# Performance work log

Measured on AMD Instinct MI355X. Metric: run time of the kernel, lower is better.

## Reference

```python
import jax, jax.numpy as jnp
import numpy as np

N = 10000
E = 160000
H = 4
NEG_SLOPE = 0.2


def _edge_softmax(e, dst):
    # e: [E, H] logits; softmax over edges sharing the same dst node
    m = jax.ops.segment_max(e, dst, num_segments=N)          # [N, H]
    m = jnp.where(jnp.isfinite(m), m, 0.0)
    ex = jnp.exp(e - m[dst])                                  # [E, H]
    den = jax.ops.segment_sum(ex, dst, num_segments=N)       # [N, H]
    return ex / (den[dst] + 1e-9)


def _gat_layer(x, src, dst, W, al, ar, resW, edge=None, We=None, ae=None):
    # x: [N, Fin]; W: [Fin, H, D]; al/ar/ae: [H, D]; resW: [Fin, D]
    feat = jnp.einsum('ni,ihd->nhd', x, W)                    # [N, H, D]
    el = jnp.einsum('nhd,hd->nh', feat, al)                   # [N, H]
    er = jnp.einsum('nhd,hd->nh', feat, ar)                   # [N, H]
    e = el[src] + er[dst]                                     # [E, H]
    if edge is not None:
        ef = jnp.einsum('ei,ihd->ehd', edge, We)              # [E, H, D]
        e = e + jnp.einsum('ehd,hd->eh', ef, ae)
    e = jax.nn.leaky_relu(e, NEG_SLOPE)
    alpha = _edge_softmax(e, dst)                             # [E, H]
    msg = feat[src] * alpha[:, :, None]                       # [E, H, D]
    out = jax.ops.segment_sum(msg, dst, num_segments=N)      # [N, H, D]
    return out.mean(axis=1) + x @ resW                        # [N, D]


def setup_inputs() -> dict:
    key = jax.random.key(0)
    ks = jax.random.split(key, 24)
    node_in, edge_in, hid, out = 128, 64, 128, 256
    s = 0.1
    d = {
        'node_feats': jax.random.normal(ks[0], (N, node_in), jnp.float32),
        'edge_feats': jax.random.normal(ks[1], (E, edge_in), jnp.float32),
        'src': jax.random.randint(ks[2], (E,), 0, N, jnp.int32),
        'dst': jax.random.randint(ks[3], (E,), 0, N, jnp.int32),
        # conv1 (with edge feats): node_in -> hid
        'W1':  s * jax.random.normal(ks[4],  (node_in, H, hid), jnp.float32),
        'We1': s * jax.random.normal(ks[5],  (edge_in, H, hid), jnp.float32),
        'al1': s * jax.random.normal(ks[6],  (H, hid), jnp.float32),
        'ar1': s * jax.random.normal(ks[7],  (H, hid), jnp.float32),
        'ae1': s * jax.random.normal(ks[8],  (H, hid), jnp.float32),
        'res1': s * jax.random.normal(ks[9], (node_in, hid), jnp.float32),
        # conv2: hid -> hid
        'W2':  s * jax.random.normal(ks[10], (hid, H, hid), jnp.float32),
        'al2': s * jax.random.normal(ks[11], (H, hid), jnp.float32),
        'ar2': s * jax.random.normal(ks[12], (H, hid), jnp.float32),
        'res2': s * jax.random.normal(ks[13], (hid, hid), jnp.float32),
        # conv3: hid -> hid
        'W3':  s * jax.random.normal(ks[14], (hid, H, hid), jnp.float32),
        'al3': s * jax.random.normal(ks[15], (H, hid), jnp.float32),
        'ar3': s * jax.random.normal(ks[16], (H, hid), jnp.float32),
        'res3': s * jax.random.normal(ks[17], (hid, hid), jnp.float32),
        # conv4: hid -> out
        'W4':  s * jax.random.normal(ks[18], (hid, H, out), jnp.float32),
        'al4': s * jax.random.normal(ks[19], (H, out), jnp.float32),
        'ar4': s * jax.random.normal(ks[20], (H, out), jnp.float32),
        'res4': s * jax.random.normal(ks[21], (hid, out), jnp.float32),
    }
    return d


def reference(node_feats, edge_feats, src, dst,
              W1, We1, al1, ar1, ae1, res1,
              W2, al2, ar2, res2,
              W3, al3, ar3, res3,
              W4, al4, ar4, res4):
    h = jax.nn.relu(_gat_layer(node_feats, src, dst, W1, al1, ar1, res1,
                               edge=edge_feats, We=We1, ae=ae1))
    h = jax.nn.relu(_gat_layer(h, src, dst, W2, al2, ar2, res2))
    h = jax.nn.relu(_gat_layer(h, src, dst, W3, al3, ar3, res3))
    h = jax.nn.relu(_gat_layer(h, src, dst, W4, al4, ar4, res4))
    return h
```

## Files before the change

### kernel.cpp

```cpp
#include <hip/hip_runtime.h>

#define NN 10000
#define EE 160000

typedef __attribute__((ext_vector_type(8))) short bf16x8;
typedef __attribute__((ext_vector_type(4))) float f32x4;
typedef __attribute__((ext_vector_type(2))) float f32x2;

__device__ __forceinline__ float b2f(unsigned short s) {
    union { unsigned u; float f; } v; v.u = ((unsigned)s) << 16; return v.f;
}
__device__ __forceinline__ short f2b(float f) {
    union { float f; unsigned u; } v; v.f = f;
    unsigned r = v.u + 0x7FFF + ((v.u >> 16) & 1);
    return (short)(r >> 16);
}
__device__ __forceinline__ unsigned char f2q(float f) {
    return (unsigned char)(__builtin_amdgcn_cvt_pk_fp8_f32(f, f, 0, false) & 0xFF);
}

__global__ __launch_bounds__(256) void hist_kernel(const int* __restrict__ dst,
                                                   int* __restrict__ counts, int E) {
    int e = blockIdx.x * 256 + threadIdx.x;
    if (e < E) atomicAdd(&counts[dst[e]], 1);
}

__global__ __launch_bounds__(256) void scan_kernel(const int* __restrict__ counts,
                                                   int* __restrict__ off,
                                                   int* __restrict__ cur, int n) {
    __shared__ int buf[NN];
    __shared__ int part[256];
    int tid = threadIdx.x;
    for (int j = tid; j < n; j += 256) buf[j] = counts[j];
    __syncthreads();
    int chunk = (n + 255) / 256;
    int lo = tid * chunk; if (lo > n) lo = n;
    int hi = lo + chunk;  if (hi > n) hi = n;
    int s = 0;
    for (int i = lo; i < hi; ++i) s += buf[i];
    part[tid] = s;
    __syncthreads();
    for (int o = 1; o < 256; o <<= 1) {
        int v = (tid >= o) ? part[tid - o] : 0;
        __syncthreads();
        part[tid] += v;
        __syncthreads();
    }
    int run = (tid == 0) ? 0 : part[tid - 1];
    for (int i = lo; i < hi; ++i) { int c = buf[i]; buf[i] = run; run += c; }
    __syncthreads();
    for (int j = tid; j < n; j += 256) { int v = buf[j]; off[j] = v; cur[j] = v; }
    if (tid == 255) off[n] = part[255];
}

__global__ __launch_bounds__(256) void fill_extra(const int* __restrict__ src,
                                                  const int* __restrict__ dst,
                                                  int* __restrict__ cur,
                                                  const float* __restrict__ ef,
                                                  const float* __restrict__ vbuf,
                                                  int* __restrict__ ssrc,
                                                  float* __restrict__ extra, int E) {
    __shared__ float vs[256];
    vs[threadIdx.x] = vbuf[threadIdx.x];
    __syncthreads();
    int e = blockIdx.x * 256 + threadIdx.x;
    if (e >= E) return;
    int p = atomicAdd(&cur[dst[e]], 1);
    ssrc[p] = src[e];
    float a0 = 0.f, a1 = 0.f, a2 = 0.f, a3 = 0.f;
    const float4* e4 = (const float4*)(ef + (size_t)e * 64);
    #pragma unroll
    for (int c = 0; c < 16; ++c) {
        float4 x = e4[c];
        int b = c * 16;
        a0 += x.x * vs[b + 0] + x.y * vs[b + 4] + x.z * vs[b + 8] + x.w * vs[b + 12];
        a1 += x.x * vs[b + 1] + x.y * vs[b + 5] + x.z * vs[b + 9] + x.w * vs[b + 13];
        a2 += x.x * vs[b + 2] + x.y * vs[b + 6] + x.z * vs[b + 10] + x.w * vs[b + 14];
        a3 += x.x * vs[b + 3] + x.y * vs[b + 7] + x.z * vs[b + 11] + x.w * vs[b + 15];
    }
    float4 o; o.x = a0; o.y = a1; o.z = a2; o.w = a3;
    *(float4*)(extra + (size_t)p * 4) = o;
}

struct PrepParams {
    const float* tsrc[8];
    short* tdst[8];
    int tN[8];
    int tshift[8];
    int tcum4[9];
    const float* W[4]; const float* al[4]; const float* ar[4];
    short* Wc[4]; int Dl[4]; int base[4];
    const float* We1; const float* ae1; float* vbuf;
    const float* node_feats; short* xb;
    int* counts;
    int bWA, bV, bC, bZ;
};
__global__ __launch_bounds__(256) void prep_kernel(PrepParams P) {
    int blk = blockIdx.x, tid = threadIdx.x;
    if (blk < P.bWA) {
        int t = blk * 256 + tid;
        if (t >= P.tcum4[8]) return;
        int i = 0;
        #pragma unroll
        for (int j = 1; j < 8; ++j) i += (t >= P.tcum4[j]);
        int local = t - P.tcum4[i];
        int N = P.tN[i], sh = P.tshift[i];
        int k = local >> (sh - 2);
        int nq = local & ((N >> 2) - 1);
        float4 v = *(const float4*)(P.tsrc[i] + (size_t)k * N + nq * 4);
        short* d = P.tdst[i] + (size_t)nq * 4 * 128 + k;
        d[0] = f2b(v.x); d[128] = f2b(v.y); d[256] = f2b(v.z); d[384] = f2b(v.w);
    } else if (blk < P.bV) {
        int bl = blk - P.bWA;
        int l = bl >> 7, within = bl & 127;
        int wv = tid >> 6, ln = tid & 63;
        int wid = within * 4 + wv;
        int k = wid >> 2, h = wid & 3;
        int D = P.Dl[l];
        const float* w = P.W[l] + ((size_t)k * 4 + h) * D;
        const float* a = P.al[l] + (size_t)h * D;
        const float* r = P.ar[l] + (size_t)h * D;
        float sa, sr;
        if (D == 128) {
            float2 w2 = ((const float2*)w)[ln];
            float2 a2 = ((const float2*)a)[ln];
            float2 r2 = ((const float2*)r)[ln];
            sa = w2.x * a2.x + w2.y * a2.y;
            sr = w2.x * r2.x + w2.y * r2.y;
        } else {
            float4 w4 = ((const float4*)w)[ln];
            float4 a4 = ((const float4*)a)[ln];
            float4 r4 = ((const float4*)r)[ln];
            sa = w4.x * a4.x + w4.y * a4.y + w4.z * a4.z + w4.w * a4.w;
            sr = w4.x * r4.x + w4.y * r4.y + w4.z * r4.z + w4.w * r4.w;
        }
        #pragma unroll
        for (int o = 32; o; o >>= 1) { sa += __shfl_xor(sa, o); sr += __shfl_xor(sr, o); }
        if (ln == 0) {
            P.Wc[l][(size_t)(P.base[l] + h) * 128 + k]     = f2b(sa);
            P.Wc[l][(size_t)(P.base[l] + 4 + h) * 128 + k] = f2b(sr);
        }
    } else if (blk < P.bC) {
        int bl = blk - P.bV;
        int wv = tid >> 6, ln = tid & 63;
        int i = bl * 4 + wv;
        #pragma unroll
        for (int h = 0; h < 4; ++h) {
            const float* w = P.We1 + ((size_t)i * 4 + h) * 128;
            const float* a = P.ae1 + (size_t)h * 128;
            float2 w2 = ((const float2*)w)[ln];
            float2 a2 = ((const float2*)a)[ln];
            float s = w2.x * a2.x + w2.y * a2.y;
            #pragma unroll
            for (int o = 32; o; o >>= 1) s += __shfl_xor(s, o);
            if (ln == 0) P.vbuf[i * 4 + h] = s;
        }
    } else if (blk < P.bZ) {
        int t = (blk - P.bC) * 256 + tid;
        if (t < NN * 32) {
            float4 v = ((const float4*)P.node_feats)[t];
            uint2 pk;
            pk.x = (unsigned short)f2b(v.x) | ((unsigned)(unsigned short)f2b(v.y) << 16);
            pk.y = (unsigned short)f2b(v.z) | ((unsigned)(unsigned short)f2b(v.w) << 16);
            ((uint2*)P.xb)[t] = pk;
        }
    } else {
        int t = (blk - P.bZ) * 256 + tid;
        if (t < NN / 4) ((int4*)P.counts)[t] = make_int4(0, 0, 0, 0);
    }
}

template <int D>
__global__ __launch_bounds__(256) void gemm_fused(const short* __restrict__ A,
                                                  const short* __restrict__ Bt,
                                                  unsigned char* __restrict__ featq,
                                                  float* __restrict__ y,
                                                  float* __restrict__ elr,
                                                  int M) {
    constexpr int HD = 4 * D;
    int wave = threadIdx.x >> 6, lane = threadIdx.x & 63;
    int m0 = blockIdx.y * 64;
    int n0 = blockIdx.x * 64 + wave * 16;
    int r = lane & 15, quad = lane >> 4;
    f32x4 acc[4] = {};
    const short* bp = Bt + (size_t)(n0 + r) * 128 + quad * 8;
    #pragma unroll
    for (int k0 = 0; k0 < 128; k0 += 32) {
        bf16x8 bfrag = *(const bf16x8*)(bp + k0);
        #pragma unroll
        for (int mt = 0; mt < 4; ++mt) {
            int gm = m0 + mt * 16 + r;
            bf16x8 afrag = {};
            if (gm < M) afrag = *(const bf16x8*)(A + (size_t)gm * 128 + k0 + quad * 8);
            acc[mt] = __builtin_amdgcn_mfma_f32_16x16x32_bf16(afrag, bfrag, acc[mt], 0, 0, 0);
        }
    }
    int col = n0 + r;
    #pragma unroll
    for (int mt = 0; mt < 4; ++mt) {
        #pragma unroll
        for (int rr = 0; rr < 4; ++rr) {
            int gm = m0 + mt * 16 + quad * 4 + rr;
            if (gm >= M) continue;
            float v = acc[mt][rr];
            if (col < HD)              featq[(size_t)gm * HD + col] = f2q(v);
            else if (col < HD + D)     y[(size_t)gm * D + (col - HD)] = v;
            else if (col < HD + D + 8) elr[(size_t)gm * 8 + (col - HD - D)] = v;
        }
    }
}

__device__ __forceinline__ void accum16q(float* a, uint4 v, float w) {
    f32x2 p;
    p = __builtin_amdgcn_cvt_pk_f32_fp8(v.x, false); a[0] += w * p.x; a[1] += w * p.y;
    p = __builtin_amdgcn_cvt_pk_f32_fp8(v.x, true);  a[2] += w * p.x; a[3] += w * p.y;
    p = __builtin_amdgcn_cvt_pk_f32_fp8(v.y, false); a[4] += w * p.x; a[5] += w * p.y;
    p = __builtin_amdgcn_cvt_pk_f32_fp8(v.y, true);  a[6] += w * p.x; a[7] += w * p.y;
    p = __builtin_amdgcn_cvt_pk_f32_fp8(v.z, false); a[8] += w * p.x; a[9] += w * p.y;
    p = __builtin_amdgcn_cvt_pk_f32_fp8(v.z, true);  a[10] += w * p.x; a[11] += w * p.y;
    p = __builtin_amdgcn_cvt_pk_f32_fp8(v.w, false); a[12] += w * p.x; a[13] += w * p.y;
    p = __builtin_amdgcn_cvt_pk_f32_fp8(v.w, true);  a[14] += w * p.x; a[15] += w * p.y;
}

__device__ __forceinline__ float hsel(int h, float s0, float s1, float s2, float s3) {
    return h == 0 ? s0 : h == 1 ? s1 : h == 2 ? s2 : s3;
}

__device__ __forceinline__ void gather128(int T, int deg, int g, int h, int sidx,
                                          float e0, float e1, float e2, float e3,
                                          const unsigned char* __restrict__ basep,
                                          float acc[16]) {
    int it = 0;
    for (; it + 4 <= T; it += 4) {
        int j0 = 2 * it + g, j1 = j0 + 2, j2 = j0 + 4, j3 = j0 + 6;
        int c0 = j0 < deg ? j0 : deg - 1;
        int c1 = j1 < deg ? j1 : deg - 1;
        int c2 = j2 < deg ? j2 : deg - 1;
        int c3 = j3 < deg ? j3 : deg - 1;
        float m0 = j0 < deg ? 1.f : 0.f, m1 = j1 < deg ? 1.f : 0.f;
        float m2 = j2 < deg ? 1.f : 0.f, m3 = j3 < deg ? 1.f : 0.f;
        int s0 = __shfl(sidx, c0), s1 = __shfl(sidx, c1);
        int s2 = __shfl(sidx, c2), s3 = __shfl(sidx, c3);
        uint4 v0 = *(const uint4*)(basep + (size_t)s0 * 512);
        uint4 v1 = *(const uint4*)(basep + (size_t)s1 * 512);
        uint4 v2 = *(const uint4*)(basep + (size_t)s2 * 512);
        uint4 v3 = *(const uint4*)(basep + (size_t)s3 * 512);
        float w0 = hsel(h, __shfl(e0, c0), __shfl(e1, c0), __shfl(e2, c0), __shfl(e3, c0)) * m0;
        float w1 = hsel(h, __shfl(e0, c1), __shfl(e1, c1), __shfl(e2, c1), __shfl(e3, c1)) * m1;
        float w2 = hsel(h, __shfl(e0, c2), __shfl(e1, c2), __shfl(e2, c2), __shfl(e3, c2)) * m2;
        float w3 = hsel(h, __shfl(e0, c3), __shfl(e1, c3), __shfl(e2, c3), __shfl(e3, c3)) * m3;
        accum16q(acc, v0, w0); accum16q(acc, v1, w1);
        accum16q(acc, v2, w2); accum16q(acc, v3, w3);
    }
    for (; it < T; ++it) {
        int j0 = 2 * it + g;
        int c0 = j0 < deg ? j0 : deg - 1;
        float m0 = j0 < deg ? 1.f : 0.f;
        int s0 = __shfl(sidx, c0);
        uint4 v0 = *(const uint4*)(basep + (size_t)s0 * 512);
        float w0 = hsel(h, __shfl(e0, c0), __shfl(e1, c0), __shfl(e2, c0), __shfl(e3, c0)) * m0;
        accum16q(acc, v0, w0);
    }
}

__device__ __forceinline__ void gather256(int T, int deg, int half, int h, int sidx,
                                          float e0, float e1, float e2, float e3,
                                          const unsigned char* __restrict__ basep,
                                          float acc[16]) {
    int it = 0;
    for (; it + 4 <= T; it += 4) {
        int j0 = 2 * it + half, j1 = j0 + 2, j2 = j0 + 4, j3 = j0 + 6;
        int c0 = j0 < deg ? j0 : deg - 1;
        int c1 = j1 < deg ? j1 : deg - 1;
        int c2 = j2 < deg ? j2 : deg - 1;
        int c3 = j3 < deg ? j3 : deg - 1;
        float m0 = j0 < deg ? 1.f : 0.f, m1 = j1 < deg ? 1.f : 0.f;
        float m2 = j2 < deg ? 1.f : 0.f, m3 = j3 < deg ? 1.f : 0.f;
        int s0 = __shfl(sidx, c0), s1 = __shfl(sidx, c1);
        int s2 = __shfl(sidx, c2), s3 = __shfl(sidx, c3);
        uint4 v0 = *(const uint4*)(basep + (size_t)s0 * 1024);
        uint4 v1 = *(const uint4*)(basep + (size_t)s1 * 1024);
        uint4 v2 = *(const uint4*)(basep + (size_t)s2 * 1024);
        uint4 v3 = *(const uint4*)(basep + (size_t)s3 * 1024);
        float w0 = hsel(h, __shfl(e0, c0), __shfl(e1, c0), __shfl(e2, c0), __shfl(e3, c0)) * m0;
        float w1 = hsel(h, __shfl(e0, c1), __shfl(e1, c1), __shfl(e2, c1), __shfl(e3, c1)) * m1;
        float w2 = hsel(h, __shfl(e0, c2), __shfl(e1, c2), __shfl(e2, c2), __shfl(e3, c2)) * m2;
        float w3 = hsel(h, __shfl(e0, c3), __shfl(e1, c3), __shfl(e2, c3), __shfl(e3, c3)) * m3;
        accum16q(acc, v0, w0); accum16q(acc, v1, w1);
        accum16q(acc, v2, w2); accum16q(acc, v3, w3);
    }
    for (; it < T; ++it) {
        int j0 = 2 * it + half;
        int c0 = j0 < deg ? j0 : deg - 1;
        float m0 = j0 < deg ? 1.f : 0.f;
        int s0 = __shfl(sidx, c0);
        uint4 v0 = *(const uint4*)(basep + (size_t)s0 * 1024);
        float w0 = hsel(h, __shfl(e0, c0), __shfl(e1, c0), __shfl(e2, c0), __shfl(e3, c0)) * m0;
        accum16q(acc, v0, w0);
    }
}

#define WAVE_MAX4(m0,m1,m2,m3)                                              \
    _Pragma("unroll")                                                       \
    for (int o = 32; o; o >>= 1) {                                          \
        m0 = fmaxf(m0, __shfl_xor(m0, o)); m1 = fmaxf(m1, __shfl_xor(m1, o));\
        m2 = fmaxf(m2, __shfl_xor(m2, o)); m3 = fmaxf(m3, __shfl_xor(m3, o));\
    }
#define WAVE_SUM4(s0,s1,s2,s3)                                              \
    _Pragma("unroll")                                                       \
    for (int o = 32; o; o >>= 1) {                                          \
        s0 += __shfl_xor(s0, o); s1 += __shfl_xor(s1, o);                   \
        s2 += __shfl_xor(s2, o); s3 += __shfl_xor(s3, o);                   \
    }

template <bool HAS_EXTRA>
__global__ __launch_bounds__(256) void gat128(const unsigned char* __restrict__ featq,
                                              const float* __restrict__ elr,
                                              const float* __restrict__ extra,
                                              const int* __restrict__ ssrc,
                                              const int* __restrict__ off,
                                              const float* __restrict__ yres,
                                              short* __restrict__ ybf) {
    int wv = threadIdx.x >> 6, ln = threadIdx.x & 63;
    int n = blockIdx.x * 4 + wv;
    int r0 = off[n], deg = off[n + 1] - r0;
    int g = ln >> 5, l5 = ln & 31;
    int h = l5 >> 3;
    float4 erv = *(const float4*)(elr + (size_t)n * 8 + 4);
    float acc[16];
    #pragma unroll
    for (int i = 0; i < 16; ++i) acc[i] = 0.f;
    float sc0, sc1, sc2, sc3;
    const unsigned char* basep = featq + l5 * 16;

    auto logits = [&](int idx, float& a0, float& a1, float& a2, float& a3) {
        int s = ssrc[idx];
        float4 elv = *(const float4*)(elr + (size_t)s * 8);
        a0 = elv.x + erv.x; a1 = elv.y + erv.y; a2 = elv.z + erv.z; a3 = elv.w + erv.w;
        if (HAS_EXTRA) {
            float4 exv = *(const float4*)(extra + (size_t)idx * 4);
            a0 += exv.x; a1 += exv.y; a2 += exv.z; a3 += exv.w;
        }
        a0 = a0 > 0.f ? a0 : 0.2f * a0;
        a1 = a1 > 0.f ? a1 : 0.2f * a1;
        a2 = a2 > 0.f ? a2 : 0.2f * a2;
        a3 = a3 > 0.f ? a3 : 0.2f * a3;
        return s;
    };

    if (deg <= 64) {
        int sidx = 0;
        float a0 = -1e30f, a1 = -1e30f, a2 = -1e30f, a3 = -1e30f;
        if (ln < deg) sidx = logits(r0 + ln, a0, a1, a2, a3);
        float m0 = a0, m1 = a1, m2 = a2, m3 = a3;
        WAVE_MAX4(m0, m1, m2, m3)
        float e0 = 0.f, e1 = 0.f, e2 = 0.f, e3 = 0.f;
        if (ln < deg) {
            e0 = __expf(a0 - m0); e1 = __expf(a1 - m1);
            e2 = __expf(a2 - m2); e3 = __expf(a3 - m3);
        }
        float s0 = e0, s1 = e1, s2 = e2, s3 = e3;
        WAVE_SUM4(s0, s1, s2, s3)
        sc0 = 0.25f / (s0 + 1e-9f); sc1 = 0.25f / (s1 + 1e-9f);
        sc2 = 0.25f / (s2 + 1e-9f); sc3 = 0.25f / (s3 + 1e-9f);
        gather128((deg + 1) >> 1, deg, g, h, sidx, e0, e1, e2, e3, basep, acc);
    } else {
        float m0 = -1e30f, m1 = -1e30f, m2 = -1e30f, m3 = -1e30f;
        for (int b = 0; b < deg; b += 64) {
            float a0 = -1e30f, a1 = -1e30f, a2 = -1e30f, a3 = -1e30f;
            if (b + ln < deg) logits(r0 + b + ln, a0, a1, a2, a3);
            m0 = fmaxf(m0, a0); m1 = fmaxf(m1, a1); m2 = fmaxf(m2, a2); m3 = fmaxf(m3, a3);
        }
        WAVE_MAX4(m0, m1, m2, m3)
        float s0 = 0.f, s1 = 0.f, s2 = 0.f, s3 = 0.f;
        for (int b = 0; b < deg; b += 64) {
            float a0, a1, a2, a3;
            if (b + ln < deg) {
                logits(r0 + b + ln, a0, a1, a2, a3);
                s0 += __expf(a0 - m0); s1 += __expf(a1 - m1);
                s2 += __expf(a2 - m2); s3 += __expf(a3 - m3);
            }
        }
        WAVE_SUM4(s0, s1, s2, s3)
        sc0 = 0.25f / (s0 + 1e-9f); sc1 = 0.25f / (s1 + 1e-9f);
        sc2 = 0.25f / (s2 + 1e-9f); sc3 = 0.25f / (s3 + 1e-9f);
        for (int b = 0; b < deg; b += 64) {
            int sidx = 0;
            float e0 = 0.f, e1 = 0.f, e2 = 0.f, e3 = 0.f;
            if (b + ln < deg) {
                float a0, a1, a2, a3;
                sidx = logits(r0 + b + ln, a0, a1, a2, a3);
                e0 = __expf(a0 - m0); e1 = __expf(a1 - m1);
                e2 = __expf(a2 - m2); e3 = __expf(a3 - m3);
            }
            int cnt = deg - b; if (cnt > 64) cnt = 64;
            gather128((cnt + 1) >> 1, cnt, g, h, sidx, e0, e1, e2, e3, basep, acc);
        }
    }

    float scl = hsel(h, sc0, sc1, sc2, sc3);
    float t[16];
    #pragma unroll
    for (int i = 0; i < 16; ++i) {
        float v = acc[i] * scl;
        v += __shfl_xor(v, 32);
        v += __shfl_xor(v, 8);
        v += __shfl_xor(v, 16);
        t[i] = v;
    }
    if (ln < 8) {
        int d0 = ln * 16;
        const float* yr = yres + (size_t)n * 128 + d0;
        unsigned pk[8];
        #pragma unroll
        for (int q = 0; q < 8; ++q) {
            float ya = yr[2 * q], yb = yr[2 * q + 1];
            float o0 = fmaxf(ya + t[2 * q], 0.f);
            float o1 = fmaxf(yb + t[2 * q + 1], 0.f);
            pk[q] = (unsigned short)f2b(o0) | ((unsigned)(unsigned short)f2b(o1) << 16);
        }
        uint4 pa, pb;
        pa.x = pk[0]; pa.y = pk[1]; pa.z = pk[2]; pa.w = pk[3];
        pb.x = pk[4]; pb.y = pk[5]; pb.z = pk[6]; pb.w = pk[7];
        *(uint4*)(ybf + (size_t)n * 128 + d0) = pa;
        *(uint4*)(ybf + (size_t)n * 128 + d0 + 8) = pb;
    }
}

__global__ __launch_bounds__(256) void gat256(const unsigned char* __restrict__ featq,
                                              const float* __restrict__ elr,
                                              const int* __restrict__ ssrc,
                                              const int* __restrict__ off,
                                              const float* __restrict__ yres,
                                              float* __restrict__ yout) {
    __shared__ float red[2][256];
    int wv = threadIdx.x >> 6, ln = threadIdx.x & 63;
    int slot = wv >> 1, half = wv & 1;
    int n = blockIdx.x * 2 + slot;
    int r0 = off[n], deg = off[n + 1] - r0;
    int h = ln >> 4;
    float4 erv = *(const float4*)(elr + (size_t)n * 8 + 4);
    float acc[16];
    #pragma unroll
    for (int i = 0; i < 16; ++i) acc[i] = 0.f;
    float sc0, sc1, sc2, sc3;
    const unsigned char* basep = featq + ln * 16;

    auto logits = [&](int idx, float& a0, float& a1, float& a2, float& a3) {
        int s = ssrc[idx];
        float4 elv = *(const float4*)(elr + (size_t)s * 8);
        a0 = elv.x + erv.x; a1 = elv.y + erv.y; a2 = elv.z + erv.z; a3 = elv.w + erv.w;
        a0 = a0 > 0.f ? a0 : 0.2f * a0;
        a1 = a1 > 0.f ? a1 : 0.2f * a1;
        a2 = a2 > 0.f ? a2 : 0.2f * a2;
        a3 = a3 > 0.f ? a3 : 0.2f * a3;
        return s;
    };

    if (deg <= 64) {
        int sidx = 0;
        float a0 = -1e30f, a1 = -1e30f, a2 = -1e30f, a3 = -1e30f;
        if (ln < deg) sidx = logits(r0 + ln, a0, a1, a2, a3);
        float m0 = a0, m1 = a1, m2 = a2, m3 = a3;
        WAVE_MAX4(m0, m1, m2, m3)
        float e0 = 0.f, e1 = 0.f, e2 = 0.f, e3 = 0.f;
        if (ln < deg) {
            e0 = __expf(a0 - m0); e1 = __expf(a1 - m1);
            e2 = __expf(a2 - m2); e3 = __expf(a3 - m3);
        }
        float s0 = e0, s1 = e1, s2 = e2, s3 = e3;
        WAVE_SUM4(s0, s1, s2, s3)
        sc0 = 0.25f / (s0 + 1e-9f); sc1 = 0.25f / (s1 + 1e-9f);
        sc2 = 0.25f / (s2 + 1e-9f); sc3 = 0.25f / (s3 + 1e-9f);
        gather256((deg + 1) >> 1, deg, half, h, sidx, e0, e1, e2, e3, basep, acc);
    } else {
        float m0 = -1e30f, m1 = -1e30f, m2 = -1e30f, m3 = -1e30f;
        for (int b = 0; b < deg; b += 64) {
            float a0 = -1e30f, a1 = -1e30f, a2 = -1e30f, a3 = -1e30f;
            if (b + ln < deg) logits(r0 + b + ln, a0, a1, a2, a3);
            m0 = fmaxf(m0, a0); m1 = fmaxf(m1, a1); m2 = fmaxf(m2, a2); m3 = fmaxf(m3, a3);
        }
        WAVE_MAX4(m0, m1, m2, m3)
        float s0 = 0.f, s1 = 0.f, s2 = 0.f, s3 = 0.f;
        for (int b = 0; b < deg; b += 64) {
            float a0, a1, a2, a3;
            if (b + ln < deg) {
                logits(r0 + b + ln, a0, a1, a2, a3);
                s0 += __expf(a0 - m0); s1 += __expf(a1 - m1);
                s2 += __expf(a2 - m2); s3 += __expf(a3 - m3);
            }
        }
        WAVE_SUM4(s0, s1, s2, s3)
        sc0 = 0.25f / (s0 + 1e-9f); sc1 = 0.25f / (s1 + 1e-9f);
        sc2 = 0.25f / (s2 + 1e-9f); sc3 = 0.25f / (s3 + 1e-9f);
        for (int b = 0; b < deg; b += 64) {
            int sidx = 0;
            float e0 = 0.f, e1 = 0.f, e2 = 0.f, e3 = 0.f;
            if (b + ln < deg) {
                float a0, a1, a2, a3;
                sidx = logits(r0 + b + ln, a0, a1, a2, a3);
                e0 = __expf(a0 - m0); e1 = __expf(a1 - m1);
                e2 = __expf(a2 - m2); e3 = __expf(a3 - m3);
            }
            int cnt = deg - b; if (cnt > 64) cnt = 64;
            gather256((cnt + 1) >> 1, cnt, half, h, sidx, e0, e1, e2, e3, basep, acc);
        }
    }

    float scl = hsel(h, sc0, sc1, sc2, sc3);
    float t[16];
    #pragma unroll
    for (int i = 0; i < 16; ++i) {
        float v = acc[i] * scl;
        v += __shfl_xor(v, 16);
        v += __shfl_xor(v, 32);
        t[i] = v;
    }
    if (half == 1 && ln < 16) {
        #pragma unroll
        for (int i = 0; i < 16; ++i) red[slot][ln * 16 + i] = t[i];
    }
    __syncthreads();
    if (half == 0 && ln < 16) {
        int d0 = ln * 16;
        const float* yr = yres + (size_t)n * 256 + d0;
        float* yo = yout + (size_t)n * 256 + d0;
        #pragma unroll
        for (int q = 0; q < 4; ++q) {
            float4 ya = *(const float4*)(yr + 4 * q);
            float4 ov;
            ov.x = fmaxf(ya.x + t[4 * q + 0] + red[slot][d0 + 4 * q + 0], 0.f);
            ov.y = fmaxf(ya.y + t[4 * q + 1] + red[slot][d0 + 4 * q + 1], 0.f);
            ov.z = fmaxf(ya.z + t[4 * q + 2] + red[slot][d0 + 4 * q + 2], 0.f);
            ov.w = fmaxf(ya.w + t[4 * q + 3] + red[slot][d0 + 4 * q + 3], 0.f);
            *(float4*)(yo + 4 * q) = ov;
        }
    }
}

extern "C" void kernel_launch(void* const* d_in, const int* in_sizes, int n_in,
                              void* d_out, int out_size, void* d_ws, size_t ws_size,
                              hipStream_t stream) {
    const float* node_feats = (const float*)d_in[0];
    const float* edge_feats = (const float*)d_in[1];
    const int*   src        = (const int*)d_in[2];
    const int*   dst        = (const int*)d_in[3];
    const float* W1   = (const float*)d_in[4];
    const float* We1  = (const float*)d_in[5];
    const float* al1  = (const float*)d_in[6];
    const float* ar1  = (const float*)d_in[7];
    const float* ae1  = (const float*)d_in[8];
    const float* res1 = (const float*)d_in[9];
    const float* W2   = (const float*)d_in[10];
    const float* al2  = (const float*)d_in[11];
    const float* ar2  = (const float*)d_in[12];
    const float* res2 = (const float*)d_in[13];
    const float* W3   = (const float*)d_in[14];
    const float* al3  = (const float*)d_in[15];
    const float* ar3  = (const float*)d_in[16];
    const float* res3 = (const float*)d_in[17];
    const float* W4   = (const float*)d_in[18];
    const float* al4  = (const float*)d_in[19];
    const float* ar4  = (const float*)d_in[20];
    const float* res4 = (const float*)d_in[21];

    char* ws = (char*)d_ws;
    auto alloc = [&](size_t bytes) -> char* {
        char* p = ws;
        ws += (bytes + 255) & ~(size_t)255;
        return p;
    };
    int*   counts  = (int*)alloc((size_t)NN * 4);
    int*   offsets = (int*)alloc((size_t)(NN + 1) * 4);
    int*   cursor  = (int*)alloc((size_t)(NN + 1) * 4);
    int*   ssrc    = (int*)alloc((size_t)EE * 4);
    unsigned char* featq = (unsigned char*)alloc((size_t)NN * 1024);
    float* xA      = (float*)alloc((size_t)NN * 128 * 4);
    short* xb      = (short*)alloc((size_t)NN * 128 * 2);
    float* elr     = (float*)alloc((size_t)NN * 8 * 4);
    float* extra   = (float*)alloc((size_t)EE * 4 * 4);
    float* vbuf    = (float*)alloc(1024);
    short* Wc1     = (short*)alloc((size_t)704 * 128 * 2);
    short* Wc2     = (short*)alloc((size_t)704 * 128 * 2);
    short* Wc3     = (short*)alloc((size_t)704 * 128 * 2);
    short* Wc4     = (short*)alloc((size_t)1344 * 128 * 2);

    PrepParams P;
    P.tsrc[0] = W1;   P.tdst[0] = Wc1;              P.tN[0] = 512;  P.tshift[0] = 9;
    P.tsrc[1] = W2;   P.tdst[1] = Wc2;              P.tN[1] = 512;  P.tshift[1] = 9;
    P.tsrc[2] = W3;   P.tdst[2] = Wc3;              P.tN[2] = 512;  P.tshift[2] = 9;
    P.tsrc[3] = W4;   P.tdst[3] = Wc4;              P.tN[3] = 1024; P.tshift[3] = 10;
    P.tsrc[4] = res1; P.tdst[4] = Wc1 + 512 * 128;  P.tN[4] = 128;  P.tshift[4] = 7;
    P.tsrc[5] = res2; P.tdst[5] = Wc2 + 512 * 128;  P.tN[5] = 128;  P.tshift[5] = 7;
    P.tsrc[6] = res3; P.tdst[6] = Wc3 + 512 * 128;  P.tN[6] = 128;  P.tshift[6] = 7;
    P.tsrc[7] = res4; P.tdst[7] = Wc4 + 1024 * 128; P.tN[7] = 256;  P.tshift[7] = 8;
    P.tcum4[0] = 0;
    for (int i = 0; i < 8; ++i) P.tcum4[i + 1] = P.tcum4[i] + P.tN[i] * 128 / 4;
    P.W[0] = W1; P.W[1] = W2; P.W[2] = W3; P.W[3] = W4;
    P.al[0] = al1; P.al[1] = al2; P.al[2] = al3; P.al[3] = al4;
    P.ar[0] = ar1; P.ar[1] = ar2; P.ar[2] = ar3; P.ar[3] = ar4;
    P.Wc[0] = Wc1; P.Wc[1] = Wc2; P.Wc[2] = Wc3; P.Wc[3] = Wc4;
    P.Dl[0] = 128; P.Dl[1] = 128; P.Dl[2] = 128; P.Dl[3] = 256;
    P.base[0] = 640; P.base[1] = 640; P.base[2] = 640; P.base[3] = 1280;
    P.We1 = We1; P.ae1 = ae1; P.vbuf = vbuf;
    P.node_feats = node_feats; P.xb = xb;
    P.counts = counts;
    P.bWA = (P.tcum4[8] + 255) / 256;
    P.bV  = P.bWA + 512;
    P.bC  = P.bV + 16;
    P.bZ  = P.bC + (NN * 32 + 255) / 256;
    int nblk = P.bZ + (NN / 4 + 255) / 256;
    prep_kernel<<<nblk, 256, 0, stream>>>(P);

    hist_kernel<<<(EE + 255) / 256, 256, 0, stream>>>(dst, counts, EE);
    scan_kernel<<<1, 256, 0, stream>>>(counts, offsets, cursor, NN);
    fill_extra<<<(EE + 255) / 256, 256, 0, stream>>>(src, dst, cursor, edge_feats,
                                                     vbuf, ssrc, extra, EE);

    float* out = (float*)d_out;
    dim3 g128(11, (NN + 63) / 64);
    dim3 g256(21, (NN + 63) / 64);
    int gs128 = NN / 4;
    int gs256 = NN / 2;

    gemm_fused<128><<<g128, 256, 0, stream>>>(xb, Wc1, featq, xA, elr, NN);
    gat128<true><<<gs128, 256, 0, stream>>>(featq, elr, extra, ssrc, offsets, xA, xb);
    gemm_fused<128><<<g128, 256, 0, stream>>>(xb, Wc2, featq, xA, elr, NN);
    gat128<false><<<gs128, 256, 0, stream>>>(featq, elr, nullptr, ssrc, offsets, xA, xb);
    gemm_fused<128><<<g128, 256, 0, stream>>>(xb, Wc3, featq, xA, elr, NN);
    gat128<false><<<gs128, 256, 0, stream>>>(featq, elr, nullptr, ssrc, offsets, xA, xb);
    gemm_fused<256><<<g256, 256, 0, stream>>>(xb, Wc4, featq, out, elr, NN);
    gat256<<<gs256, 256, 0, stream>>>(featq, elr, ssrc, offsets, out, out);
}
```

Baseline: 364.5 us.

## Fuse histogram into first GEMM, widen per-node gather across waves, register scan

```diff
diff --git a/kernel.cpp b/kernel.cpp
--- a/kernel.cpp
+++ b/kernel.cpp
@@ -19,25 +19,27 @@
     return (unsigned char)(__builtin_amdgcn_cvt_pk_fp8_f32(f, f, 0, false) & 0xFF);
 }
 
-__global__ __launch_bounds__(256) void hist_kernel(const int* __restrict__ dst,
-                                                   int* __restrict__ counts, int E) {
-    int e = blockIdx.x * 256 + threadIdx.x;
-    if (e < E) atomicAdd(&counts[dst[e]], 1);
-}
-
 __global__ __launch_bounds__(256) void scan_kernel(const int* __restrict__ counts,
                                                    int* __restrict__ off,
                                                    int* __restrict__ cur, int n) {
-    __shared__ int buf[NN];
     __shared__ int part[256];
     int tid = threadIdx.x;
-    for (int j = tid; j < n; j += 256) buf[j] = counts[j];
-    __syncthreads();
-    int chunk = (n + 255) / 256;
-    int lo = tid * chunk; if (lo > n) lo = n;
-    int hi = lo + chunk;  if (hi > n) hi = n;
+    int lo = tid * 40;
+    int4 r[10];
     int s = 0;
-    for (int i = lo; i < hi; ++i) s += buf[i];
+    #pragma unroll
+    for (int q = 0; q < 10; ++q) {
+        int idx = lo + q * 4;
+        int4 v = make_int4(0, 0, 0, 0);
+        if (idx + 3 < n) v = *(const int4*)(counts + idx);
+        else if (idx < n) {
+            v.x = counts[idx];
+            v.y = (idx + 1 < n) ? counts[idx + 1] : 0;
+            v.z = (idx + 2 < n) ? counts[idx + 2] : 0;
+        }
+        r[q] = v;
+        s += v.x + v.y + v.z + v.w;
+    }
     part[tid] = s;
     __syncthreads();
     for (int o = 1; o < 256; o <<= 1) {
@@ -46,10 +48,22 @@
         part[tid] += v;
         __syncthreads();
     }
-    int run = (tid == 0) ? 0 : part[tid - 1];
-    for (int i = lo; i < hi; ++i) { int c = buf[i]; buf[i] = run; run += c; }
-    __syncthreads();
-    for (int j = tid; j < n; j += 256) { int v = buf[j]; off[j] = v; cur[j] = v; }
+    int run = tid ? part[tid - 1] : 0;
+    #pragma unroll
+    for (int q = 0; q < 10; ++q) {
+        int4 v = r[q], o4;
+        o4.x = run; run += v.x;
+        o4.y = run; run += v.y;
+        o4.z = run; run += v.z;
+        o4.w = run; run += v.w;
+        int idx = lo + q * 4;
+        if (idx + 3 < n) { *(int4*)(off + idx) = o4; *(int4*)(cur + idx) = o4; }
+        else if (idx < n) {
+            off[idx] = o4.x; cur[idx] = o4.x;
+            if (idx + 1 < n) { off[idx + 1] = o4.y; cur[idx + 1] = o4.y; }
+            if (idx + 2 < n) { off[idx + 2] = o4.z; cur[idx + 2] = o4.z; }
+        }
+    }
     if (tid == 255) off[n] = part[255];
 }
 
@@ -171,16 +185,16 @@
 }
 
 template <int D>
-__global__ __launch_bounds__(256) void gemm_fused(const short* __restrict__ A,
-                                                  const short* __restrict__ Bt,
-                                                  unsigned char* __restrict__ featq,
-                                                  float* __restrict__ y,
-                                                  float* __restrict__ elr,
-                                                  int M) {
+__device__ __forceinline__ void gemm_body(const short* __restrict__ A,
+                                          const short* __restrict__ Bt,
+                                          unsigned char* __restrict__ featq,
+                                          float* __restrict__ y,
+                                          float* __restrict__ elr,
+                                          int M, int bx, int by) {
     constexpr int HD = 4 * D;
     int wave = threadIdx.x >> 6, lane = threadIdx.x & 63;
-    int m0 = blockIdx.y * 64;
-    int n0 = blockIdx.x * 64 + wave * 16;
+    int m0 = by * 64;
+    int n0 = bx * 64 + wave * 16;
     int r = lane & 15, quad = lane >> 4;
     f32x4 acc[4] = {};
     const short* bp = Bt + (size_t)(n0 + r) * 128 + quad * 8;
@@ -208,6 +222,33 @@
             else if (col < HD + D + 8) elr[(size_t)gm * 8 + (col - HD - D)] = v;
         }
     }
+}
+
+template <int D>
+__global__ __launch_bounds__(256) void gemm_fused(const short* __restrict__ A,
+                                                  const short* __restrict__ Bt,
+                                                  unsigned char* __restrict__ featq,
+                                                  float* __restrict__ y,
+                                                  float* __restrict__ elr,
+                                                  int M) {
+    gemm_body<D>(A, Bt, featq, y, elr, M, blockIdx.x, blockIdx.y);
+}
+
+__global__ __launch_bounds__(256) void hist_gemm1(const int* __restrict__ dst,
+                                                  int* __restrict__ counts,
+                                                  const short* __restrict__ A,
+                                                  const short* __restrict__ Bt,
+                                                  unsigned char* __restrict__ featq,
+                                                  float* __restrict__ y,
+                                                  float* __restrict__ elr) {
+    constexpr int HB = (EE + 255) / 256;
+    if (blockIdx.x < HB) {
+        int e = blockIdx.x * 256 + threadIdx.x;
+        if (e < EE) atomicAdd(&counts[dst[e]], 1);
+        return;
+    }
+    int b = blockIdx.x - HB;
+    gemm_body<128>(A, Bt, featq, y, elr, NN, b % 11, b / 11);
 }
 
 __device__ __forceinline__ void accum16q(float* a, uint4 v, float w) {
@@ -226,13 +267,13 @@
     return h == 0 ? s0 : h == 1 ? s1 : h == 2 ? s2 : s3;
 }
 
-__device__ __forceinline__ void gather128(int T, int deg, int g, int h, int sidx,
+__device__ __forceinline__ void gather128(int T, int deg, int sub, int h, int sidx,
                                           float e0, float e1, float e2, float e3,
                                           const unsigned char* __restrict__ basep,
                                           float acc[16]) {
     int it = 0;
     for (; it + 4 <= T; it += 4) {
-        int j0 = 2 * it + g, j1 = j0 + 2, j2 = j0 + 4, j3 = j0 + 6;
+        int j0 = 4 * it + sub, j1 = j0 + 4, j2 = j0 + 8, j3 = j0 + 12;
         int c0 = j0 < deg ? j0 : deg - 1;
         int c1 = j1 < deg ? j1 : deg - 1;
         int c2 = j2 < deg ? j2 : deg - 1;
@@ -253,7 +294,7 @@
         accum16q(acc, v2, w2); accum16q(acc, v3, w3);
     }
     for (; it < T; ++it) {
-        int j0 = 2 * it + g;
+        int j0 = 4 * it + sub;
         int c0 = j0 < deg ? j0 : deg - 1;
         float m0 = j0 < deg ? 1.f : 0.f;
         int s0 = __shfl(sidx, c0);
@@ -263,13 +304,13 @@
     }
 }
 
-__device__ __forceinline__ void gather256(int T, int deg, int half, int h, int sidx,
+__device__ __forceinline__ void gather256(int T, int deg, int sub, int h, int sidx,
                                           float e0, float e1, float e2, float e3,
                                           const unsigned char* __restrict__ basep,
                                           float acc[16]) {
     int it = 0;
     for (; it + 4 <= T; it += 4) {
-        int j0 = 2 * it + half, j1 = j0 + 2, j2 = j0 + 4, j3 = j0 + 6;
+        int j0 = 4 * it + sub, j1 = j0 + 4, j2 = j0 + 8, j3 = j0 + 12;
         int c0 = j0 < deg ? j0 : deg - 1;
         int c1 = j1 < deg ? j1 : deg - 1;
         int c2 = j2 < deg ? j2 : deg - 1;
@@ -290,7 +331,7 @@
         accum16q(acc, v2, w2); accum16q(acc, v3, w3);
     }
     for (; it < T; ++it) {
-        int j0 = 2 * it + half;
+        int j0 = 4 * it + sub;
         int c0 = j0 < deg ? j0 : deg - 1;
         float m0 = j0 < deg ? 1.f : 0.f;
         int s0 = __shfl(sidx, c0);
@@ -321,8 +362,10 @@
                                               const int* __restrict__ off,
                                               const float* __restrict__ yres,
                                               short* __restrict__ ybf) {
+    __shared__ float red[2][128];
     int wv = threadIdx.x >> 6, ln = threadIdx.x & 63;
-    int n = blockIdx.x * 4 + wv;
+    int slot = wv >> 1, half = wv & 1;
+    int n = blockIdx.x * 2 + slot;
     int r0 = off[n], deg = off[n + 1] - r0;
     int g = ln >> 5, l5 = ln & 31;
     int h = l5 >> 3;
@@ -332,6 +375,7 @@
     for (int i = 0; i < 16; ++i) acc[i] = 0.f;
     float sc0, sc1, sc2, sc3;
     const unsigned char* basep = featq + l5 * 16;
+    int sub = half * 2 + g;
 
     auto logits = [&](int idx, float& a0, float& a1, float& a2, float& a3) {
         int s = ssrc[idx];
@@ -363,7 +407,7 @@
         WAVE_SUM4(s0, s1, s2, s3)
         sc0 = 0.25f / (s0 + 1e-9f); sc1 = 0.25f / (s1 + 1e-9f);
         sc2 = 0.25f / (s2 + 1e-9f); sc3 = 0.25f / (s3 + 1e-9f);
-        gather128((deg + 1) >> 1, deg, g, h, sidx, e0, e1, e2, e3, basep, acc);
+        gather128((deg + 3) >> 2, deg, sub, h, sidx, e0, e1, e2, e3, basep, acc);
     } else {
         float m0 = -1e30f, m1 = -1e30f, m2 = -1e30f, m3 = -1e30f;
         for (int b = 0; b < deg; b += 64) {
@@ -394,7 +438,7 @@
                 e2 = __expf(a2 - m2); e3 = __expf(a3 - m3);
             }
             int cnt = deg - b; if (cnt > 64) cnt = 64;
-            gather128((cnt + 1) >> 1, cnt, g, h, sidx, e0, e1, e2, e3, basep, acc);
+            gather128((cnt + 3) >> 2, cnt, sub, h, sidx, e0, e1, e2, e3, basep, acc);
         }
     }
 
@@ -408,15 +452,20 @@
         v += __shfl_xor(v, 16);
         t[i] = v;
     }
-    if (ln < 8) {
+    if (half == 1 && ln < 8) {
+        #pragma unroll
+        for (int i = 0; i < 16; ++i) red[slot][ln * 16 + i] = t[i];
+    }
+    __syncthreads();
+    if (half == 0 && ln < 8) {
         int d0 = ln * 16;
         const float* yr = yres + (size_t)n * 128 + d0;
         unsigned pk[8];
         #pragma unroll
         for (int q = 0; q < 8; ++q) {
             float ya = yr[2 * q], yb = yr[2 * q + 1];
-            float o0 = fmaxf(ya + t[2 * q], 0.f);
-            float o1 = fmaxf(yb + t[2 * q + 1], 0.f);
+            float o0 = fmaxf(ya + t[2 * q] + red[slot][d0 + 2 * q], 0.f);
+            float o1 = fmaxf(yb + t[2 * q + 1] + red[slot][d0 + 2 * q + 1], 0.f);
             pk[q] = (unsigned short)f2b(o0) | ((unsigned)(unsigned short)f2b(o1) << 16);
         }
         uint4 pa, pb;
@@ -433,10 +482,9 @@
                                               const int* __restrict__ off,
                                               const float* __restrict__ yres,
                                               float* __restrict__ yout) {
-    __shared__ float red[2][256];
+    __shared__ float red[3][256];
     int wv = threadIdx.x >> 6, ln = threadIdx.x & 63;
-    int slot = wv >> 1, half = wv & 1;
-    int n = blockIdx.x * 2 + slot;
+    int n = blockIdx.x;
     int r0 = off[n], deg = off[n + 1] - r0;
     int h = ln >> 4;
     float4 erv = *(const float4*)(elr + (size_t)n * 8 + 4);
@@ -472,7 +520,7 @@
         WAVE_SUM4(s0, s1, s2, s3)
         sc0 = 0.25f / (s0 + 1e-9f); sc1 = 0.25f / (s1 + 1e-9f);
         sc2 = 0.25f / (s2 + 1e-9f); sc3 = 0.25f / (s3 + 1e-9f);
-        gather256((deg + 1) >> 1, deg, half, h, sidx, e0, e1, e2, e3, basep, acc);
+        gather256((deg + 3) >> 2, deg, wv, h, sidx, e0, e1, e2, e3, basep, acc);
     } else {
         float m0 = -1e30f, m1 = -1e30f, m2 = -1e30f, m3 = -1e30f;
         for (int b = 0; b < deg; b += 64) {
@@ -503,7 +551,7 @@
                 e2 = __expf(a2 - m2); e3 = __expf(a3 - m3);
             }
             int cnt = deg - b; if (cnt > 64) cnt = 64;
-            gather256((cnt + 1) >> 1, cnt, half, h, sidx, e0, e1, e2, e3, basep, acc);
+            gather256((cnt + 3) >> 2, cnt, wv, h, sidx, e0, e1, e2, e3, basep, acc);
         }
     }
 
@@ -516,12 +564,12 @@
         v += __shfl_xor(v, 32);
         t[i] = v;
     }
-    if (half == 1 && ln < 16) {
-        #pragma unroll
-        for (int i = 0; i < 16; ++i) red[slot][ln * 16 + i] = t[i];
+    if (wv > 0 && ln < 16) {
+        #pragma unroll
+        for (int i = 0; i < 16; ++i) red[wv - 1][ln * 16 + i] = t[i];
     }
     __syncthreads();
-    if (half == 0 && ln < 16) {
+    if (wv == 0 && ln < 16) {
         int d0 = ln * 16;
         const float* yr = yres + (size_t)n * 256 + d0;
         float* yo = yout + (size_t)n * 256 + d0;
@@ -529,10 +577,10 @@
         for (int q = 0; q < 4; ++q) {
             float4 ya = *(const float4*)(yr + 4 * q);
             float4 ov;
-            ov.x = fmaxf(ya.x + t[4 * q + 0] + red[slot][d0 + 4 * q + 0], 0.f);
-            ov.y = fmaxf(ya.y + t[4 * q + 1] + red[slot][d0 + 4 * q + 1], 0.f);
-            ov.z = fmaxf(ya.z + t[4 * q + 2] + red[slot][d0 + 4 * q + 2], 0.f);
-            ov.w = fmaxf(ya.w + t[4 * q + 3] + red[slot][d0 + 4 * q + 3], 0.f);
+            ov.x = fmaxf(ya.x + t[4 * q + 0] + red[0][d0 + 4 * q + 0] + red[1][d0 + 4 * q + 0] + red[2][d0 + 4 * q + 0], 0.f);
+            ov.y = fmaxf(ya.y + t[4 * q + 1] + red[0][d0 + 4 * q + 1] + red[1][d0 + 4 * q + 1] + red[2][d0 + 4 * q + 1], 0.f);
+            ov.z = fmaxf(ya.z + t[4 * q + 2] + red[0][d0 + 4 * q + 2] + red[1][d0 + 4 * q + 2] + red[2][d0 + 4 * q + 2], 0.f);
+            ov.w = fmaxf(ya.w + t[4 * q + 3] + red[0][d0 + 4 * q + 3] + red[1][d0 + 4 * q + 3] + red[2][d0 + 4 * q + 3], 0.f);
             *(float4*)(yo + 4 * q) = ov;
         }
     }
@@ -612,23 +660,22 @@
     int nblk = P.bZ + (NN / 4 + 255) / 256;
     prep_kernel<<<nblk, 256, 0, stream>>>(P);
 
-    hist_kernel<<<(EE + 255) / 256, 256, 0, stream>>>(dst, counts, EE);
+    float* out = (float*)d_out;
+    dim3 g128(11, (NN + 63) / 64);
+    dim3 g256(21, (NN + 63) / 64);
+    constexpr int HB = (EE + 255) / 256;
+
+    hist_gemm1<<<HB + 11 * ((NN + 63) / 64), 256, 0, stream>>>(dst, counts, xb, Wc1,
+                                                               featq, xA, elr);
     scan_kernel<<<1, 256, 0, stream>>>(counts, offsets, cursor, NN);
     fill_extra<<<(EE + 255) / 256, 256, 0, stream>>>(src, dst, cursor, edge_feats,
                                                      vbuf, ssrc, extra, EE);
 
-    float* out = (float*)d_out;
-    dim3 g128(11, (NN + 63) / 64);
-    dim3 g256(21, (NN + 63) / 64);
-    int gs128 = NN / 4;
-    int gs256 = NN / 2;
-
-    gemm_fused<128><<<g128, 256, 0, stream>>>(xb, Wc1, featq, xA, elr, NN);
-    gat128<true><<<gs128, 256, 0, stream>>>(featq, elr, extra, ssrc, offsets, xA, xb);
+    gat128<true><<<NN / 2, 256, 0, stream>>>(featq, elr, extra, ssrc, offsets, xA, xb);
     gemm_fused<128><<<g128, 256, 0, stream>>>(xb, Wc2, featq, xA, elr, NN);
-    gat128<false><<<gs128, 256, 0, stream>>>(featq, elr, nullptr, ssrc, offsets, xA, xb);
+    gat128<false><<<NN / 2, 256, 0, stream>>>(featq, elr, nullptr, ssrc, offsets, xA, xb);
     gemm_fused<128><<<g128, 256, 0, stream>>>(xb, Wc3, featq, xA, elr, NN);
-    gat128<false><<<gs128, 256, 0, stream>>>(featq, elr, nullptr, ssrc, offsets, xA, xb);
+    gat128<false><<<NN / 2, 256, 0, stream>>>(featq, elr, nullptr, ssrc, offsets, xA, xb);
     gemm_fused<256><<<g256, 256, 0, stream>>>(xb, Wc4, featq, out, elr, NN);
-    gat256<<<gs256, 256, 0, stream>>>(featq, elr, ssrc, offsets, out, out);
-}
+    gat256<<<NN, 256, 0, stream>>>(featq, elr, ssrc, offsets, out, out);
+}
```

Result: slower. 414.7 us (+13.8%).
